# Kernel optimization log

Measured on AMD Instinct MI355X. Metric: run time of the kernel, lower is better.

Reference implementation:

```python
import jax, jax.numpy as jnp
import numpy as np

TOPK = 4
ROUTE_SCALE = 1.0


def setup_inputs() -> dict:
    key = jax.random.key(0)
    ks = jax.random.split(key, 16)
    B, S, C, D = 4, 512, 4, 2048
    E, H = 16, 1408
    SH = 2 * H  # n_shared_experts * moe_inter_dim
    s = 0.02
    return {
        "embeddings": jax.random.normal(ks[0], (B, S, C, D), jnp.float32),
        "x": jax.random.normal(ks[1], (B, S, C, 1), jnp.float32),
        "Wg": jax.random.normal(ks[2], (E, D), jnp.float32) * s,
        "W1": jax.random.normal(ks[3], (E, H, D), jnp.float32) * s,
        "b1": jax.random.normal(ks[4], (E, H), jnp.float32) * s,
        "W2": jax.random.normal(ks[5], (E, D, H), jnp.float32) * s,
        "b2": jax.random.normal(ks[6], (E, D), jnp.float32) * s,
        "W3": jax.random.normal(ks[7], (E, H, D), jnp.float32) * s,
        "b3": jax.random.normal(ks[8], (E, H), jnp.float32) * s,
        "Ws1": jax.random.normal(ks[9], (SH, D), jnp.float32) * s,
        "bs1": jax.random.normal(ks[10], (SH,), jnp.float32) * s,
        "Ws2": jax.random.normal(ks[11], (D, SH), jnp.float32) * s,
        "bs2": jax.random.normal(ks[12], (D,), jnp.float32) * s,
    }


def reference(embeddings, x, Wg, W1, b1, W2, b2, W3, b3, Ws1, bs1, Ws2, bs2):
    # NOTE: in the torch module, the `x` arg is immediately shadowed by
    # embeddings.view(-1, dim); it does not participate in the math.
    D = Wg.shape[1]
    E = Wg.shape[0]
    xt = embeddings.reshape(-1, D)  # [N, D] flattened tokens

    # Gate: softmax scores (fp32), top-k routing; n_groups == 1, no gate bias.
    logits = jnp.einsum("nd,ed->ne", xt, Wg)
    scores = jax.nn.softmax(logits.astype(jnp.float32), axis=-1)  # [N, E]
    topv, idx = jax.lax.top_k(scores, TOPK)  # values == gathered original scores
    weights = (topv * ROUTE_SCALE).astype(xt.dtype)  # [N, K]

    # Expert dispatch/combine. Per-token combined weight for expert e is
    # sum_k weights[n, k] * (idx[n, k] == e); unassigned tokens get weight 0,
    # so masked-dense per-expert SwiGLU reproduces the gather/scatter math.
    y = jnp.zeros_like(xt)
    for e in range(E):
        w_e = jnp.sum(weights * (idx == e).astype(weights.dtype), axis=1)  # [N]
        h = jax.nn.silu(xt @ W1[e].T + b1[e]) * (xt @ W3[e].T + b3[e])  # [N, H]
        y = y + (h @ W2[e].T + b2[e]) * w_e[:, None]

    # Shared experts: Linear -> SiLU -> Linear applied to every token.
    z = jax.nn.silu(xt @ Ws1.T + bs1) @ Ws2.T + bs2

    return (y + z).reshape(embeddings.shape)
```

## Files before the change

kernel.cpp:

```cpp
#include <hip/hip_runtime.h>
#include <stdint.h>

#define N_TOK 8192
#define DIM   2048
#define NEXP  16
#define HID   1408
#define SHID  2816
#define KTOP  4
#define TILEMAX 272

typedef __attribute__((ext_vector_type(8))) short bf16x8;
typedef __attribute__((ext_vector_type(4))) float f32x4;

#define MFMA16(a,b,c) __builtin_amdgcn_mfma_f32_16x16x32_bf16((a),(b),(c),0,0,0)

__device__ __forceinline__ unsigned short f2b(float f){
  unsigned u = __float_as_uint(f);
  return (unsigned short)((u + 0x7fffu + ((u >> 16) & 1u)) >> 16);
}
__device__ __forceinline__ unsigned pk2(float a, float b){
  return (unsigned)f2b(a) | ((unsigned)f2b(b) << 16);
}
__device__ __forceinline__ float bu2f(unsigned hs){ return __uint_as_float(hs << 16); }
__device__ __forceinline__ float siluf(float x){ return x / (1.f + expf(-x)); }
__device__ __forceinline__ f32x4 zero4(){ f32x4 z; z[0]=0.f; z[1]=0.f; z[2]=0.f; z[3]=0.f; return z; }

__device__ __forceinline__ void gll16(const unsigned short* g, unsigned short* l){
  __builtin_amdgcn_global_load_lds(
      (const __attribute__((address_space(1))) void*)g,
      (__attribute__((address_space(3))) void*)l, 16, 0, 0);
}

__global__ __launch_bounds__(256) void k_cvt(const float* __restrict__ s,
                                             unsigned short* __restrict__ d, size_t n4){
  size_t i = (size_t)blockIdx.x*256 + threadIdx.x;
  size_t st = (size_t)gridDim.x*256;
  for (; i < n4; i += st){
    float4 v = ((const float4*)s)[i];
    uint2 q; q.x = pk2(v.x, v.y); q.y = pk2(v.z, v.w);
    ((uint2*)d)[i] = q;
  }
}

__global__ __launch_bounds__(256) void k_gate(const float* __restrict__ X, const float* __restrict__ Wg,
                                              float* __restrict__ topw, int* __restrict__ topi,
                                              int* __restrict__ cnt){
  int lane = threadIdx.x & 63;
  int t = blockIdx.x*4 + (threadIdx.x >> 6);
  const float* xr = X + (size_t)t*DIM;
  float xv[32];
#pragma unroll
  for (int i=0;i<32;i++) xv[i] = xr[i*64 + lane];
  float sc[NEXP];
#pragma unroll
  for (int e=0;e<NEXP;e++){
    const float* wr = Wg + e*DIM;
    float s = 0.f;
#pragma unroll
    for (int i=0;i<32;i++) s = fmaf(xv[i], wr[i*64 + lane], s);
#pragma unroll
    for (int d=1; d<64; d<<=1) s += __shfl_xor(s, d);
    sc[e] = s;
  }
  if (lane == 0){
    float m = sc[0];
#pragma unroll
    for (int e=1;e<NEXP;e++) m = fmaxf(m, sc[e]);
    float den = 0.f;
#pragma unroll
    for (int e=0;e<NEXP;e++){ sc[e] = expf(sc[e]-m); den += sc[e]; }
    float inv = 1.f/den;
#pragma unroll
    for (int e=0;e<NEXP;e++) sc[e] *= inv;
    for (int k=0;k<KTOP;k++){
      int bi = 0; float bv = sc[0];
#pragma unroll
      for (int e=1;e<NEXP;e++) if (sc[e] > bv){ bv = sc[e]; bi = e; }
      topw[t*KTOP+k] = bv;
      topi[t*KTOP+k] = bi;
#pragma unroll
      for (int e=0;e<NEXP;e++) if (e == bi) sc[e] = -1.f;
      atomicAdd(&cnt[bi], 1);
    }
  }
}

__global__ void k_scan(const int* __restrict__ cnt, int* __restrict__ off, int* __restrict__ cur,
                       int* __restrict__ tab){
  if (threadIdx.x == 0){
    int a = 0;
    for (int e=0;e<NEXP;e++){ off[e] = a; cur[e] = a; a += cnt[e]; }
    int n = 0;
    for (int e=0;e<NEXP;e++){
      int nt = (cnt[e] + 127) >> 7;
      for (int r=0;r<nt;r++) tab[n++] = (e << 16) | r;
    }
    for (; n < TILEMAX; ++n) tab[n] = -1;
  }
}

__global__ __launch_bounds__(256) void k_place(const int* __restrict__ topi, const float* __restrict__ topw,
                                               int* __restrict__ cur, int* __restrict__ rows,
                                               float* __restrict__ rw, int* __restrict__ slotL){
  int t = blockIdx.x*256 + threadIdx.x;
#pragma unroll
  for (int k=0;k<KTOP;k++){
    int e = topi[t*KTOP+k];
    int p = atomicAdd(&cur[e], 1);
    rows[p] = t;
    rw[p]   = topw[t*KTOP+k];
    slotL[t*KTOP+k] = p;
  }
}

__device__ __forceinline__ void stage_Bf(unsigned short* lsB, const float* bF,
                                         int ldK, int bn0, int k0, int tid){
#pragma unroll
  for (int j=0;j<8;j++){
    int idx = j*256 + tid, r = idx >> 4, c4 = idx & 15;
    float4 v = *(const float4*)(bF + (size_t)(bn0 + r)*ldK + k0 + c4*4);
    uint2 q; q.x = pk2(v.x, v.y); q.y = pk2(v.z, v.w);
    *(uint2*)&lsB[r*64 + (((c4 >> 1) ^ (r & 7)) << 3) + ((c4 & 1) << 2)] = q;
  }
}

__device__ __forceinline__ void read_A(bf16x8 af[4], const unsigned short* lsA, int wm, int lane, int kc){
  int s = kc*4 + (lane >> 4);
#pragma unroll
  for (int mi=0;mi<4;mi++){
    int r = wm + mi*16 + (lane & 15);
    af[mi] = *(const bf16x8*)&lsA[r*64 + ((s ^ (r & 7)) << 3)];
  }
}

template<bool WBF>
__global__ __launch_bounds__(256,2) void k_g13(const unsigned short* __restrict__ Xb,
    const void* __restrict__ W1p, const void* __restrict__ W3p,
    const float* __restrict__ b1, const float* __restrict__ b3,
    const int* __restrict__ rows, const int* __restrict__ cnt, const int* __restrict__ offs,
    const int* __restrict__ tab, unsigned short* __restrict__ H1)
{
  int bid = blockIdx.x;
  int l = bid >> 3;
  int ct = l / 34;
  int slot = (bid & 7)*34 + (l - ct*34);
  int ent = tab[slot];
  if (ent < 0) return;
  int e = ent >> 16, rt = ent & 0xffff;
  int cntE = cnt[e];
  int offE = offs[e];
  int hn0 = ct*128;
  int tid = threadIdx.x, lane = tid & 63, wid = tid >> 6;
  int wm = (wid >> 1)*64, wn = (wid & 1)*64;
  __shared__ alignas(16) unsigned short lsA[8192], lsB1[8192], lsB3[8192];

  int lr8 = lane >> 3;
  int cx  = (lane & 7) ^ lr8;
  unsigned offA[4];
#pragma unroll
  for (int j=0;j<4;j++){
    int lrow = rt*128 + wid*32 + j*8 + lr8;
    int arow = rows[offE + (lrow < cntE ? lrow : cntE-1)];
    offA[j] = (unsigned)arow*DIM + (unsigned)cx*8;
  }
  unsigned offB0 = (unsigned)(hn0 + wid*32 + lr8)*DIM + (unsigned)cx*8;
  const unsigned short* b1H = (const unsigned short*)W1p + (size_t)e*HID*DIM;
  const unsigned short* b3H = (const unsigned short*)W3p + (size_t)e*HID*DIM;
  const float* b1F = (const float*)W1p + (size_t)e*HID*DIM;
  const float* b3F = (const float*)W3p + (size_t)e*HID*DIM;
  unsigned short* lA  = &lsA[wid*2048];
  unsigned short* lB1 = &lsB1[wid*2048];
  unsigned short* lB3 = &lsB3[wid*2048];

  f32x4 acc1[4][4], acc3[4][4];
#pragma unroll
  for (int i=0;i<4;i++)
#pragma unroll
    for (int j=0;j<4;j++){ acc1[i][j] = zero4(); acc3[i][j] = zero4(); }

  for (int kt=0; kt<DIM/64; ++kt){
    int k0 = kt*64;
    __syncthreads();
#pragma unroll
    for (int j=0;j<4;j++){
      gll16(Xb + offA[j] + k0, lA + j*512);
      if constexpr (WBF){
        gll16(b1H + offB0 + j*(8*DIM) + k0, lB1 + j*512);
        gll16(b3H + offB0 + j*(8*DIM) + k0, lB3 + j*512);
      }
    }
    if constexpr (!WBF){
      stage_Bf(lsB1, b1F, DIM, hn0, k0, tid);
      stage_Bf(lsB3, b3F, DIM, hn0, k0, tid);
    }
    __syncthreads();
#pragma unroll
    for (int kc=0;kc<2;kc++){
      bf16x8 af[4]; read_A(af, lsA, wm, lane, kc);
      int sB = kc*4 + (lane >> 4);
#pragma unroll
      for (int nj=0;nj<4;nj++){
        int rb = wn + nj*16 + (lane & 15);
        int lof = rb*64 + ((sB ^ (rb & 7)) << 3);
        bf16x8 bf1 = *(const bf16x8*)&lsB1[lof];
        bf16x8 bf3 = *(const bf16x8*)&lsB3[lof];
#pragma unroll
        for (int mi=0;mi<4;mi++){
          acc1[mi][nj] = MFMA16(af[mi], bf1, acc1[mi][nj]);
          acc3[mi][nj] = MFMA16(af[mi], bf3, acc3[mi][nj]);
        }
      }
    }
  }
#pragma unroll
  for (int nj=0;nj<4;nj++){
    int h = hn0 + wn + nj*16 + (lane & 15);
    float b1v = b1[e*HID + h];
    float b3v = b3[e*HID + h];
#pragma unroll
    for (int mi=0;mi<4;mi++){
#pragma unroll
      for (int r=0;r<4;r++){
        int gr = rt*128 + wm + mi*16 + (lane >> 4)*4 + r;
        if (gr < cntE){
          float u = acc1[mi][nj][r] + b1v;
          float v = acc3[mi][nj][r] + b3v;
          H1[(size_t)(offE + gr)*HID + h] = f2b(siluf(u)*v);
        }
      }
    }
  }
}

template<int MODE, bool WBF, int KSTEPS>
__global__ __launch_bounds__(256,2) void k_gemm(const unsigned short* __restrict__ Abase,
    const void* __restrict__ Bpv, const float* __restrict__ bias,
    float* __restrict__ outF, unsigned short* __restrict__ outH,
    const int* __restrict__ rows, const float* __restrict__ rw,
    const int* __restrict__ cnt, const int* __restrict__ offs,
    const int* __restrict__ tab)
{
  constexpr int KD = KSTEPS*64;
  int e = 0, ct, rt, cntE = 0, offE = 0;
  int bid = blockIdx.x;
  int l = bid >> 3;
  if constexpr (MODE >= 2){
    ct = l / 34;
    int slot = (bid & 7)*34 + (l - ct*34);
    int ent = tab[slot];
    if (ent < 0) return;
    e = ent >> 16; rt = ent & 0xffff;
    cntE = cnt[e];
    offE = offs[e];
  } else {
    rt = (bid & 7)*8 + (l & 7);
    ct = l >> 3;
  }
  int bn0 = ct*128, t0 = rt*128;
  int tid = threadIdx.x, lane = tid & 63, wid = tid >> 6;
  int wm = (wid >> 1)*64, wn = (wid & 1)*64;
  __shared__ alignas(16) unsigned short lsA[8192], lsB[8192];

  int lr8 = lane >> 3;
  int cx  = (lane & 7) ^ lr8;
  unsigned offA0 = 0;
  unsigned offA[4];
  if constexpr (MODE >= 2){
#pragma unroll
    for (int j=0;j<4;j++){
      int lrow = t0 + wid*32 + j*8 + lr8;
      int arow = offE + (lrow < cntE ? lrow : cntE-1);
      offA[j] = (unsigned)arow*KD + (unsigned)cx*8;
    }
  } else {
    offA0 = (unsigned)(t0 + wid*32 + lr8)*KD + (unsigned)cx*8;
  }
  unsigned offB0 = (unsigned)(bn0 + wid*32 + lr8)*KD + (unsigned)cx*8;
  const unsigned short* bH = (const unsigned short*)Bpv + ((MODE >= 2) ? (size_t)e*2048*KD : (size_t)0);
  const float*          bF = (const float*)Bpv          + ((MODE >= 2) ? (size_t)e*2048*KD : (size_t)0);
  const float* biasp = bias + ((MODE >= 2) ? e*DIM : 0);
  unsigned short* lA = &lsA[wid*2048];
  unsigned short* lB = &lsB[wid*2048];

  f32x4 acc[4][4];
#pragma unroll
  for (int i=0;i<4;i++)
#pragma unroll
    for (int j=0;j<4;j++) acc[i][j] = zero4();

  for (int kt=0; kt<KSTEPS; ++kt){
    int k0 = kt*64;
    __syncthreads();
#pragma unroll
    for (int j=0;j<4;j++){
      if constexpr (MODE >= 2) gll16(Abase + offA[j] + k0, lA + j*512);
      else                     gll16(Abase + offA0 + j*(8*KD) + k0, lA + j*512);
      if constexpr (WBF)       gll16(bH + offB0 + j*(8*KD) + k0, lB + j*512);
    }
    if constexpr (!WBF) stage_Bf(lsB, bF, KD, bn0, k0, tid);
    __syncthreads();
#pragma unroll
    for (int kc=0;kc<2;kc++){
      bf16x8 af[4]; read_A(af, lsA, wm, lane, kc);
      int sB = kc*4 + (lane >> 4);
#pragma unroll
      for (int nj=0;nj<4;nj++){
        int rb = wn + nj*16 + (lane & 15);
        bf16x8 bfr = *(const bf16x8*)&lsB[rb*64 + ((sB ^ (rb & 7)) << 3)];
#pragma unroll
        for (int mi=0;mi<4;mi++)
          acc[mi][nj] = MFMA16(af[mi], bfr, acc[mi][nj]);
      }
    }
  }
#pragma unroll
  for (int nj=0;nj<4;nj++){
    int col = bn0 + wn + nj*16 + (lane & 15);
    float bv = biasp[col];
#pragma unroll
    for (int mi=0;mi<4;mi++){
#pragma unroll
      for (int r=0;r<4;r++){
        int lr = wm + mi*16 + (lane >> 4)*4 + r;
        float v = acc[mi][nj][r] + bv;
        if constexpr (MODE == 0){
          outH[(size_t)(t0 + lr)*SHID + col] = f2b(siluf(v));
        } else if constexpr (MODE == 1){
          outF[(size_t)(t0 + lr)*DIM + col] = v;
        } else {
          int gr = t0 + lr;
          if (gr < cntE){
            int slot = offE + gr;
            float wv = rw[slot] * v;
            if constexpr (MODE == 2){
              atomicAdd(outF + (size_t)rows[slot]*DIM + col, wv);
            } else {
              outH[(size_t)slot*DIM + col] = f2b(wv);
            }
          }
        }
      }
    }
  }
}

__global__ __launch_bounds__(256) void k_comb(const unsigned short* __restrict__ Yr,
                                              const int* __restrict__ slotL, float* __restrict__ out){
  int i = blockIdx.x*256 + threadIdx.x;
  int t = i >> 8, c = i & 255;
  size_t ob = (size_t)t*DIM + (size_t)c*8;
  float4 a = *(float4*)(out + ob);
  float4 b = *(float4*)(out + ob + 4);
  int sl[4];
#pragma unroll
  for (int k=0;k<KTOP;k++) sl[k] = slotL[t*KTOP + k];
#pragma unroll
  for (int k=0;k<KTOP;k++){
    uint4 v = *(const uint4*)(Yr + (size_t)sl[k]*DIM + (size_t)c*8);
    a.x += bu2f(v.x & 0xffffu); a.y += bu2f(v.x >> 16);
    a.z += bu2f(v.y & 0xffffu); a.w += bu2f(v.y >> 16);
    b.x += bu2f(v.z & 0xffffu); b.y += bu2f(v.z >> 16);
    b.z += bu2f(v.w & 0xffffu); b.w += bu2f(v.w >> 16);
  }
  *(float4*)(out + ob) = a;
  *(float4*)(out + ob + 4) = b;
}

extern "C" void kernel_launch(void* const* d_in, const int* in_sizes, int n_in,
                              void* d_out, int out_size, void* d_ws, size_t ws_size,
                              hipStream_t stream)
{
  (void)in_sizes; (void)n_in; (void)out_size;
  const float* emb = (const float*)d_in[0];
  const float* Wg  = (const float*)d_in[2];
  const float* W1  = (const float*)d_in[3];
  const float* b1  = (const float*)d_in[4];
  const float* W2  = (const float*)d_in[5];
  const float* b2  = (const float*)d_in[6];
  const float* W3  = (const float*)d_in[7];
  const float* b3  = (const float*)d_in[8];
  const float* Ws1 = (const float*)d_in[9];
  const float* bs1 = (const float*)d_in[10];
  const float* Ws2 = (const float*)d_in[11];
  const float* bs2 = (const float*)d_in[12];
  float* out = (float*)d_out;
  char* ws = (char*)d_ws;

  const size_t SZ_XB = (size_t)N_TOK*DIM*2;
  const size_t SZ_H1 = (size_t)N_TOK*KTOP*HID*2;
  const size_t SZ_HS = (size_t)N_TOK*SHID*2;
  const size_t SZ_T4 = (size_t)N_TOK*KTOP*4;
  const size_t SZ_WB = (size_t)NEXP*HID*DIM*2;
  const size_t SZ_SB = (size_t)SHID*DIM*2;
  const size_t SZ_YR = (size_t)N_TOK*KTOP*DIM*2;

  size_t off_xb = 0;
  size_t off_h1 = off_xb + SZ_XB;
  size_t off_hs = off_h1 + SZ_H1;
  size_t off_tw = off_hs + SZ_HS;
  size_t off_ti = off_tw + SZ_T4;
  size_t off_ro = off_ti + SZ_T4;
  size_t off_rw = off_ro + SZ_T4;
  size_t off_sl = off_rw + SZ_T4;
  size_t off_cnt = off_sl + SZ_T4;
  size_t off_off = off_cnt + 256;
  size_t off_cur = off_off + 256;
  size_t off_tab = off_cur + 256;
  size_t base_end = off_tab + TILEMAX*4 + 64;
  size_t off_w1b = base_end;
  size_t off_w3b = off_w1b + SZ_WB;
  size_t off_w2b = off_w3b + SZ_WB;
  size_t off_s1b = off_w2b + SZ_WB;
  size_t off_s2b = off_s1b + SZ_SB;
  size_t wbf_end = off_s2b + SZ_SB;

  bool wbf = ws_size >= wbf_end;
  size_t off_yr = wbf ? wbf_end : base_end;
  bool comb = ws_size >= off_yr + SZ_YR;

  unsigned short* Xb = (unsigned short*)(ws + off_xb);
  unsigned short* H1 = (unsigned short*)(ws + off_h1);
  unsigned short* Hs = (unsigned short*)(ws + off_hs);
  float* topw = (float*)(ws + off_tw);
  int*   topi = (int*)(ws + off_ti);
  int*   rowsL= (int*)(ws + off_ro);
  float* rwL  = (float*)(ws + off_rw);
  int*   slotL= (int*)(ws + off_sl);
  int*   cntP = (int*)(ws + off_cnt);
  int*   offP = (int*)(ws + off_off);
  int*   curP = (int*)(ws + off_cur);
  int*   tabP = (int*)(ws + off_tab);
  unsigned short* Yr = (unsigned short*)(ws + off_yr);

  hipMemsetAsync(ws + off_cnt, 0, 768, stream);
  k_cvt<<<2048, 256, 0, stream>>>(emb, Xb, (size_t)N_TOK*DIM/4);
  if (wbf){
    k_cvt<<<2048, 256, 0, stream>>>(W1,  (unsigned short*)(ws + off_w1b), (size_t)NEXP*HID*DIM/4);
    k_cvt<<<2048, 256, 0, stream>>>(W3,  (unsigned short*)(ws + off_w3b), (size_t)NEXP*HID*DIM/4);
    k_cvt<<<2048, 256, 0, stream>>>(W2,  (unsigned short*)(ws + off_w2b), (size_t)NEXP*HID*DIM/4);
    k_cvt<<<512,  256, 0, stream>>>(Ws1, (unsigned short*)(ws + off_s1b), (size_t)SHID*DIM/4);
    k_cvt<<<512,  256, 0, stream>>>(Ws2, (unsigned short*)(ws + off_s2b), (size_t)SHID*DIM/4);
  }
  k_gate<<<2048, 256, 0, stream>>>(emb, Wg, topw, topi, cntP);
  k_scan<<<1, 64, 0, stream>>>(cntP, offP, curP, tabP);
  k_place<<<32, 256, 0, stream>>>(topi, topw, curP, rowsL, rwL, slotL);

  if (wbf) k_g13<true ><<<2992, 256, 0, stream>>>(Xb, ws+off_w1b, ws+off_w3b, b1, b3, rowsL, cntP, offP, tabP, H1);
  else     k_g13<false><<<2992, 256, 0, stream>>>(Xb, W1, W3, b1, b3, rowsL, cntP, offP, tabP, H1);

  if (wbf) k_gemm<0,true ,32><<<1408, 256, 0, stream>>>(Xb, ws+off_s1b, bs1, nullptr, Hs, nullptr,nullptr,nullptr,nullptr,nullptr);
  else     k_gemm<0,false,32><<<1408, 256, 0, stream>>>(Xb, Ws1, bs1, nullptr, Hs, nullptr,nullptr,nullptr,nullptr,nullptr);

  if (wbf) k_gemm<1,true ,44><<<1024, 256, 0, stream>>>(Hs, ws+off_s2b, bs2, out, nullptr, nullptr,nullptr,nullptr,nullptr,nullptr);
  else     k_gemm<1,false,44><<<1024, 256, 0, stream>>>(Hs, Ws2, bs2, out, nullptr, nullptr,nullptr,nullptr,nullptr,nullptr);

  if (comb){
    if (wbf) k_gemm<3,true ,22><<<4352, 256, 0, stream>>>(H1, ws+off_w2b, b2, nullptr, Yr, rowsL, rwL, cntP, offP, tabP);
    else     k_gemm<3,false,22><<<4352, 256, 0, stream>>>(H1, W2, b2, nullptr, Yr, rowsL, rwL, cntP, offP, tabP);
    k_comb<<<N_TOK, 256, 0, stream>>>(Yr, slotL, out);
  } else {
    if (wbf) k_gemm<2,true ,22><<<4352, 256, 0, stream>>>(H1, ws+off_w2b, b2, out, nullptr, rowsL, rwL, cntP, offP, tabP);
    else     k_gemm<2,false,22><<<4352, 256, 0, stream>>>(H1, W2, b2, out, nullptr, rowsL, rwL, cntP, offP, tabP);
  }
}
```

Measured before the change: 1.768 ms.

## Double-buffer LDS staging in expert GEMMs and fuse weight conversion launches

```diff
diff --git a/kernel.cpp b/kernel.cpp
--- a/kernel.cpp
+++ b/kernel.cpp
@@ -39,6 +39,28 @@
     float4 v = ((const float4*)s)[i];
     uint2 q; q.x = pk2(v.x, v.y); q.y = pk2(v.z, v.w);
     ((uint2*)d)[i] = q;
+  }
+}
+
+#define SEGW ((size_t)NEXP*HID*DIM/4)
+#define SEGS ((size_t)SHID*DIM/4)
+__global__ __launch_bounds__(256) void k_cvtW(const float* __restrict__ W1, const float* __restrict__ W3,
+                                              const float* __restrict__ W2, const float* __restrict__ Ws1,
+                                              const float* __restrict__ Ws2,
+                                              unsigned short* __restrict__ d1, unsigned short* __restrict__ d3,
+                                              unsigned short* __restrict__ d2, unsigned short* __restrict__ ds1,
+                                              unsigned short* __restrict__ ds2){
+  size_t total = 3*SEGW + 2*SEGS;
+  for (size_t i = (size_t)blockIdx.x*256 + threadIdx.x; i < total; i += (size_t)gridDim.x*256){
+    const float* s; unsigned short* d; size_t off;
+    if      (i <   SEGW)        { s = W1;  d = d1;  off = i; }
+    else if (i < 2*SEGW)        { s = W3;  d = d3;  off = i - SEGW; }
+    else if (i < 3*SEGW)        { s = W2;  d = d2;  off = i - 2*SEGW; }
+    else if (i < 3*SEGW + SEGS) { s = Ws1; d = ds1; off = i - 3*SEGW; }
+    else                        { s = Ws2; d = ds2; off = i - 3*SEGW - SEGS; }
+    float4 v = ((const float4*)s)[off];
+    uint2 q; q.x = pk2(v.x, v.y); q.y = pk2(v.z, v.w);
+    ((uint2*)d)[off] = q;
   }
 }
 
@@ -124,12 +146,33 @@
   }
 }
 
+__device__ __forceinline__ void stage_Bf32(unsigned short* lsB, const float* bF,
+                                           int bn0, int k0, int tid){
+#pragma unroll
+  for (int j=0;j<4;j++){
+    int idx = j*256 + tid;
+    int r = idx >> 3, c4 = idx & 7;
+    float4 v = *(const float4*)(bF + (size_t)(bn0 + r)*DIM + k0 + c4*4);
+    uint2 q; q.x = pk2(v.x, v.y); q.y = pk2(v.z, v.w);
+    *(uint2*)&lsB[r*32 + (((c4 >> 1) ^ ((r >> 1) & 3)) << 3) + ((c4 & 1) << 2)] = q;
+  }
+}
+
 __device__ __forceinline__ void read_A(bf16x8 af[4], const unsigned short* lsA, int wm, int lane, int kc){
   int s = kc*4 + (lane >> 4);
 #pragma unroll
   for (int mi=0;mi<4;mi++){
     int r = wm + mi*16 + (lane & 15);
     af[mi] = *(const bf16x8*)&lsA[r*64 + ((s ^ (r & 7)) << 3)];
+  }
+}
+
+__device__ __forceinline__ void read_A32(bf16x8 af[4], const unsigned short* lsA, int wm, int lane){
+  int s = lane >> 4;
+#pragma unroll
+  for (int mi=0;mi<4;mi++){
+    int r = wm + mi*16 + (lane & 15);
+    af[mi] = *(const bf16x8*)&lsA[r*32 + ((s ^ ((r >> 1) & 3)) << 3)];
   }
 }
 
@@ -152,25 +195,24 @@
   int hn0 = ct*128;
   int tid = threadIdx.x, lane = tid & 63, wid = tid >> 6;
   int wm = (wid >> 1)*64, wn = (wid & 1)*64;
-  __shared__ alignas(16) unsigned short lsA[8192], lsB1[8192], lsB3[8192];
-
-  int lr8 = lane >> 3;
-  int cx  = (lane & 7) ^ lr8;
-  unsigned offA[4];
-#pragma unroll
-  for (int j=0;j<4;j++){
-    int lrow = rt*128 + wid*32 + j*8 + lr8;
+  __shared__ alignas(16) unsigned short lsA[2][4096], lsB1[2][4096], lsB3[2][4096];
+
+  int r0 = tid >> 2;
+  int sl = tid & 3;
+  int cxg = sl ^ ((r0 >> 1) & 3);
+  unsigned offA[2];
+#pragma unroll
+  for (int j=0;j<2;j++){
+    int lrow = rt*128 + r0 + j*64;
     int arow = rows[offE + (lrow < cntE ? lrow : cntE-1)];
-    offA[j] = (unsigned)arow*DIM + (unsigned)cx*8;
-  }
-  unsigned offB0 = (unsigned)(hn0 + wid*32 + lr8)*DIM + (unsigned)cx*8;
+    offA[j] = (unsigned)arow*DIM + (unsigned)cxg*8;
+  }
+  unsigned offB0 = (unsigned)(hn0 + r0)*DIM + (unsigned)cxg*8;
   const unsigned short* b1H = (const unsigned short*)W1p + (size_t)e*HID*DIM;
   const unsigned short* b3H = (const unsigned short*)W3p + (size_t)e*HID*DIM;
   const float* b1F = (const float*)W1p + (size_t)e*HID*DIM;
   const float* b3F = (const float*)W3p + (size_t)e*HID*DIM;
-  unsigned short* lA  = &lsA[wid*2048];
-  unsigned short* lB1 = &lsB1[wid*2048];
-  unsigned short* lB3 = &lsB3[wid*2048];
+  unsigned dst0 = (unsigned)tid*8;
 
   f32x4 acc1[4][4], acc3[4][4];
 #pragma unroll
@@ -178,39 +220,42 @@
 #pragma unroll
     for (int j=0;j<4;j++){ acc1[i][j] = zero4(); acc3[i][j] = zero4(); }
 
-  for (int kt=0; kt<DIM/64; ++kt){
-    int k0 = kt*64;
+  auto STAGE = [&](int set, int k0){
+#pragma unroll
+    for (int j=0;j<2;j++){
+      gll16(Xb + offA[j] + k0, &lsA[set][dst0 + j*2048]);
+      if constexpr (WBF){
+        gll16(b1H + offB0 + j*(64*DIM) + k0, &lsB1[set][dst0 + j*2048]);
+        gll16(b3H + offB0 + j*(64*DIM) + k0, &lsB3[set][dst0 + j*2048]);
+      }
+    }
+    if constexpr (!WBF){
+      stage_Bf32(lsB1[set], b1F, hn0, k0, tid);
+      stage_Bf32(lsB3[set], b3F, hn0, k0, tid);
+    }
+  };
+
+  STAGE(0, 0);
+  __syncthreads();
+  int cur = 0;
+  for (int kt=0; kt<DIM/32; ++kt){
+    if (kt+1 < DIM/32) STAGE(cur^1, (kt+1)*32);
+    bf16x8 af[4]; read_A32(af, lsA[cur], wm, lane);
+    int s = lane >> 4;
+#pragma unroll
+    for (int nj=0;nj<4;nj++){
+      int rb = wn + nj*16 + (lane & 15);
+      int lof = rb*32 + ((s ^ ((rb >> 1) & 3)) << 3);
+      bf16x8 bf1 = *(const bf16x8*)&lsB1[cur][lof];
+      bf16x8 bf3 = *(const bf16x8*)&lsB3[cur][lof];
+#pragma unroll
+      for (int mi=0;mi<4;mi++){
+        acc1[mi][nj] = MFMA16(af[mi], bf1, acc1[mi][nj]);
+        acc3[mi][nj] = MFMA16(af[mi], bf3, acc3[mi][nj]);
+      }
+    }
     __syncthreads();
-#pragma unroll
-    for (int j=0;j<4;j++){
-      gll16(Xb + offA[j] + k0, lA + j*512);
-      if constexpr (WBF){
-        gll16(b1H + offB0 + j*(8*DIM) + k0, lB1 + j*512);
-        gll16(b3H + offB0 + j*(8*DIM) + k0, lB3 + j*512);
-      }
-    }
-    if constexpr (!WBF){
-      stage_Bf(lsB1, b1F, DIM, hn0, k0, tid);
-      stage_Bf(lsB3, b3F, DIM, hn0, k0, tid);
-    }
-    __syncthreads();
-#pragma unroll
-    for (int kc=0;kc<2;kc++){
-      bf16x8 af[4]; read_A(af, lsA, wm, lane, kc);
-      int sB = kc*4 + (lane >> 4);
-#pragma unroll
-      for (int nj=0;nj<4;nj++){
-        int rb = wn + nj*16 + (lane & 15);
-        int lof = rb*64 + ((sB ^ (rb & 7)) << 3);
-        bf16x8 bf1 = *(const bf16x8*)&lsB1[lof];
-        bf16x8 bf3 = *(const bf16x8*)&lsB3[lof];
-#pragma unroll
-        for (int mi=0;mi<4;mi++){
-          acc1[mi][nj] = MFMA16(af[mi], bf1, acc1[mi][nj]);
-          acc3[mi][nj] = MFMA16(af[mi], bf3, acc3[mi][nj]);
-        }
-      }
-    }
+    cur ^= 1;
   }
 #pragma unroll
   for (int nj=0;nj<4;nj++){
@@ -259,7 +304,7 @@
   int bn0 = ct*128, t0 = rt*128;
   int tid = threadIdx.x, lane = tid & 63, wid = tid >> 6;
   int wm = (wid >> 1)*64, wn = (wid & 1)*64;
-  __shared__ alignas(16) unsigned short lsA[8192], lsB[8192];
+  __shared__ alignas(16) unsigned short lsA[2][8192], lsB[2][8192];
 
   int lr8 = lane >> 3;
   int cx  = (lane & 7) ^ lr8;
@@ -279,8 +324,6 @@
   const unsigned short* bH = (const unsigned short*)Bpv + ((MODE >= 2) ? (size_t)e*2048*KD : (size_t)0);
   const float*          bF = (const float*)Bpv          + ((MODE >= 2) ? (size_t)e*2048*KD : (size_t)0);
   const float* biasp = bias + ((MODE >= 2) ? e*DIM : 0);
-  unsigned short* lA = &lsA[wid*2048];
-  unsigned short* lB = &lsB[wid*2048];
 
   f32x4 acc[4][4];
 #pragma unroll
@@ -288,30 +331,36 @@
 #pragma unroll
     for (int j=0;j<4;j++) acc[i][j] = zero4();
 
+  auto STAGE = [&](int set, int k0){
+#pragma unroll
+    for (int j=0;j<4;j++){
+      if constexpr (MODE >= 2) gll16(Abase + offA[j] + k0, &lsA[set][wid*2048 + j*512]);
+      else                     gll16(Abase + offA0 + j*(8*KD) + k0, &lsA[set][wid*2048 + j*512]);
+      if constexpr (WBF)       gll16(bH + offB0 + j*(8*KD) + k0, &lsB[set][wid*2048 + j*512]);
+    }
+    if constexpr (!WBF) stage_Bf(lsB[set], bF, KD, bn0, k0, tid);
+  };
+
+  STAGE(0, 0);
+  __syncthreads();
+  int cur = 0;
   for (int kt=0; kt<KSTEPS; ++kt){
-    int k0 = kt*64;
-    __syncthreads();
-#pragma unroll
-    for (int j=0;j<4;j++){
-      if constexpr (MODE >= 2) gll16(Abase + offA[j] + k0, lA + j*512);
-      else                     gll16(Abase + offA0 + j*(8*KD) + k0, lA + j*512);
-      if constexpr (WBF)       gll16(bH + offB0 + j*(8*KD) + k0, lB + j*512);
-    }
-    if constexpr (!WBF) stage_Bf(lsB, bF, KD, bn0, k0, tid);
-    __syncthreads();
+    if (kt+1 < KSTEPS) STAGE(cur^1, (kt+1)*64);
 #pragma unroll
     for (int kc=0;kc<2;kc++){
-      bf16x8 af[4]; read_A(af, lsA, wm, lane, kc);
+      bf16x8 af[4]; read_A(af, lsA[cur], wm, lane, kc);
       int sB = kc*4 + (lane >> 4);
 #pragma unroll
       for (int nj=0;nj<4;nj++){
         int rb = wn + nj*16 + (lane & 15);
-        bf16x8 bfr = *(const bf16x8*)&lsB[rb*64 + ((sB ^ (rb & 7)) << 3)];
+        bf16x8 bfr = *(const bf16x8*)&lsB[cur][rb*64 + ((sB ^ (rb & 7)) << 3)];
 #pragma unroll
         for (int mi=0;mi<4;mi++)
           acc[mi][nj] = MFMA16(af[mi], bfr, acc[mi][nj]);
       }
     }
+    __syncthreads();
+    cur ^= 1;
   }
 #pragma unroll
   for (int nj=0;nj<4;nj++){
@@ -435,11 +484,10 @@
   hipMemsetAsync(ws + off_cnt, 0, 768, stream);
   k_cvt<<<2048, 256, 0, stream>>>(emb, Xb, (size_t)N_TOK*DIM/4);
   if (wbf){
-    k_cvt<<<2048, 256, 0, stream>>>(W1,  (unsigned short*)(ws + off_w1b), (size_t)NEXP*HID*DIM/4);
-    k_cvt<<<2048, 256, 0, stream>>>(W3,  (unsigned short*)(ws + off_w3b), (size_t)NEXP*HID*DIM/4);
-    k_cvt<<<2048, 256, 0, stream>>>(W2,  (unsigned short*)(ws + off_w2b), (size_t)NEXP*HID*DIM/4);
-    k_cvt<<<512,  256, 0, stream>>>(Ws1, (unsigned short*)(ws + off_s1b), (size_t)SHID*DIM/4);
-    k_cvt<<<512,  256, 0, stream>>>(Ws2, (unsigned short*)(ws + off_s2b), (size_t)SHID*DIM/4);
+    k_cvtW<<<4096, 256, 0, stream>>>(W1, W3, W2, Ws1, Ws2,
+        (unsigned short*)(ws + off_w1b), (unsigned short*)(ws + off_w3b),
+        (unsigned short*)(ws + off_w2b), (unsigned short*)(ws + off_s1b),
+        (unsigned short*)(ws + off_s2b));
   }
   k_gate<<<2048, 256, 0, stream>>>(emb, Wg, topw, topi, cntP);
   k_scan<<<1, 64, 0, stream>>>(cntP, offP, curP, tabP);
```

New measurement: 2.079 ms. 17.6% more time.

## Widen GEMM N-tile to 256, fuse X conversion into gate, merge weight casts

Applied to the files above, without the earlier changes.

```diff
diff --git a/kernel.cpp b/kernel.cpp
--- a/kernel.cpp
+++ b/kernel.cpp
@@ -31,33 +31,52 @@
       (__attribute__((address_space(3))) void*)l, 16, 0, 0);
 }
 
-__global__ __launch_bounds__(256) void k_cvt(const float* __restrict__ s,
-                                             unsigned short* __restrict__ d, size_t n4){
-  size_t i = (size_t)blockIdx.x*256 + threadIdx.x;
-  size_t st = (size_t)gridDim.x*256;
-  for (; i < n4; i += st){
-    float4 v = ((const float4*)s)[i];
+#define SEGW ((size_t)NEXP*HID*DIM/4)
+#define SEGS ((size_t)SHID*DIM/4)
+__global__ __launch_bounds__(256) void k_cvtW(const float* __restrict__ W1, const float* __restrict__ W3,
+                                              const float* __restrict__ W2, const float* __restrict__ Ws1,
+                                              const float* __restrict__ Ws2,
+                                              unsigned short* __restrict__ d1, unsigned short* __restrict__ d3,
+                                              unsigned short* __restrict__ d2, unsigned short* __restrict__ ds1,
+                                              unsigned short* __restrict__ ds2){
+  size_t total = 3*SEGW + 2*SEGS;
+  for (size_t i = (size_t)blockIdx.x*256 + threadIdx.x; i < total; i += (size_t)gridDim.x*256){
+    const float* s; unsigned short* d; size_t off;
+    if      (i <   SEGW)        { s = W1;  d = d1;  off = i; }
+    else if (i < 2*SEGW)        { s = W3;  d = d3;  off = i - SEGW; }
+    else if (i < 3*SEGW)        { s = W2;  d = d2;  off = i - 2*SEGW; }
+    else if (i < 3*SEGW + SEGS) { s = Ws1; d = ds1; off = i - 3*SEGW; }
+    else                        { s = Ws2; d = ds2; off = i - 3*SEGW - SEGS; }
+    float4 v = ((const float4*)s)[off];
     uint2 q; q.x = pk2(v.x, v.y); q.y = pk2(v.z, v.w);
-    ((uint2*)d)[i] = q;
+    ((uint2*)d)[off] = q;
   }
 }
 
 __global__ __launch_bounds__(256) void k_gate(const float* __restrict__ X, const float* __restrict__ Wg,
                                               float* __restrict__ topw, int* __restrict__ topi,
-                                              int* __restrict__ cnt){
+                                              int* __restrict__ cnt, unsigned short* __restrict__ Xb){
   int lane = threadIdx.x & 63;
   int t = blockIdx.x*4 + (threadIdx.x >> 6);
   const float* xr = X + (size_t)t*DIM;
-  float xv[32];
-#pragma unroll
-  for (int i=0;i<32;i++) xv[i] = xr[i*64 + lane];
+  float4 xv[8];
+#pragma unroll
+  for (int i=0;i<8;i++){
+    xv[i] = *(const float4*)(xr + i*256 + lane*4);
+    uint2 q; q.x = pk2(xv[i].x, xv[i].y); q.y = pk2(xv[i].z, xv[i].w);
+    *(uint2*)(Xb + (size_t)t*DIM + i*256 + lane*4) = q;
+  }
   float sc[NEXP];
 #pragma unroll
   for (int e=0;e<NEXP;e++){
     const float* wr = Wg + e*DIM;
     float s = 0.f;
 #pragma unroll
-    for (int i=0;i<32;i++) s = fmaf(xv[i], wr[i*64 + lane], s);
+    for (int i=0;i<8;i++){
+      float4 w = *(const float4*)(wr + i*256 + lane*4);
+      s = fmaf(xv[i].x, w.x, s); s = fmaf(xv[i].y, w.y, s);
+      s = fmaf(xv[i].z, w.z, s); s = fmaf(xv[i].w, w.w, s);
+    }
 #pragma unroll
     for (int d=1; d<64; d<<=1) s += __shfl_xor(s, d);
     sc[e] = s;
@@ -113,10 +132,11 @@
   }
 }
 
+template<int ROUNDS>
 __device__ __forceinline__ void stage_Bf(unsigned short* lsB, const float* bF,
                                          int ldK, int bn0, int k0, int tid){
 #pragma unroll
-  for (int j=0;j<8;j++){
+  for (int j=0;j<ROUNDS;j++){
     int idx = j*256 + tid, r = idx >> 4, c4 = idx & 15;
     float4 v = *(const float4*)(bF + (size_t)(bn0 + r)*ldK + k0 + c4*4);
     uint2 q; q.x = pk2(v.x, v.y); q.y = pk2(v.z, v.w);
@@ -190,8 +210,8 @@
       }
     }
     if constexpr (!WBF){
-      stage_Bf(lsB1, b1F, DIM, hn0, k0, tid);
-      stage_Bf(lsB3, b3F, DIM, hn0, k0, tid);
+      stage_Bf<8>(lsB1, b1F, DIM, hn0, k0, tid);
+      stage_Bf<8>(lsB3, b3F, DIM, hn0, k0, tid);
     }
     __syncthreads();
 #pragma unroll
@@ -256,10 +276,10 @@
     rt = (bid & 7)*8 + (l & 7);
     ct = l >> 3;
   }
-  int bn0 = ct*128, t0 = rt*128;
+  int bn0 = ct*256, t0 = rt*128;
   int tid = threadIdx.x, lane = tid & 63, wid = tid >> 6;
-  int wm = (wid >> 1)*64, wn = (wid & 1)*64;
-  __shared__ alignas(16) unsigned short lsA[8192], lsB[8192];
+  int wm = (wid >> 1)*64, wn = (wid & 1)*128;
+  __shared__ alignas(16) unsigned short lsA[8192], lsB[16384];
 
   int lr8 = lane >> 3;
   int cx  = (lane & 7) ^ lr8;
@@ -275,18 +295,18 @@
   } else {
     offA0 = (unsigned)(t0 + wid*32 + lr8)*KD + (unsigned)cx*8;
   }
-  unsigned offB0 = (unsigned)(bn0 + wid*32 + lr8)*KD + (unsigned)cx*8;
+  unsigned offB0 = (unsigned)(bn0 + wid*64 + lr8)*KD + (unsigned)cx*8;
   const unsigned short* bH = (const unsigned short*)Bpv + ((MODE >= 2) ? (size_t)e*2048*KD : (size_t)0);
   const float*          bF = (const float*)Bpv          + ((MODE >= 2) ? (size_t)e*2048*KD : (size_t)0);
   const float* biasp = bias + ((MODE >= 2) ? e*DIM : 0);
   unsigned short* lA = &lsA[wid*2048];
-  unsigned short* lB = &lsB[wid*2048];
-
-  f32x4 acc[4][4];
+  unsigned short* lB = &lsB[wid*4096];
+
+  f32x4 acc[4][8];
 #pragma unroll
   for (int i=0;i<4;i++)
 #pragma unroll
-    for (int j=0;j<4;j++) acc[i][j] = zero4();
+    for (int j=0;j<8;j++) acc[i][j] = zero4();
 
   for (int kt=0; kt<KSTEPS; ++kt){
     int k0 = kt*64;
@@ -295,16 +315,20 @@
     for (int j=0;j<4;j++){
       if constexpr (MODE >= 2) gll16(Abase + offA[j] + k0, lA + j*512);
       else                     gll16(Abase + offA0 + j*(8*KD) + k0, lA + j*512);
-      if constexpr (WBF)       gll16(bH + offB0 + j*(8*KD) + k0, lB + j*512);
-    }
-    if constexpr (!WBF) stage_Bf(lsB, bF, KD, bn0, k0, tid);
+    }
+    if constexpr (WBF){
+#pragma unroll
+      for (int j=0;j<8;j++) gll16(bH + offB0 + j*(8*KD) + k0, lB + j*512);
+    } else {
+      stage_Bf<16>(lsB, bF, KD, bn0, k0, tid);
+    }
     __syncthreads();
 #pragma unroll
     for (int kc=0;kc<2;kc++){
       bf16x8 af[4]; read_A(af, lsA, wm, lane, kc);
       int sB = kc*4 + (lane >> 4);
 #pragma unroll
-      for (int nj=0;nj<4;nj++){
+      for (int nj=0;nj<8;nj++){
         int rb = wn + nj*16 + (lane & 15);
         bf16x8 bfr = *(const bf16x8*)&lsB[rb*64 + ((sB ^ (rb & 7)) << 3)];
 #pragma unroll
@@ -314,7 +338,7 @@
     }
   }
 #pragma unroll
-  for (int nj=0;nj<4;nj++){
+  for (int nj=0;nj<8;nj++){
     int col = bn0 + wn + nj*16 + (lane & 15);
     float bv = biasp[col];
 #pragma unroll
@@ -433,33 +457,31 @@
   unsigned short* Yr = (unsigned short*)(ws + off_yr);
 
   hipMemsetAsync(ws + off_cnt, 0, 768, stream);
-  k_cvt<<<2048, 256, 0, stream>>>(emb, Xb, (size_t)N_TOK*DIM/4);
   if (wbf){
-    k_cvt<<<2048, 256, 0, stream>>>(W1,  (unsigned short*)(ws + off_w1b), (size_t)NEXP*HID*DIM/4);
-    k_cvt<<<2048, 256, 0, stream>>>(W3,  (unsigned short*)(ws + off_w3b), (size_t)NEXP*HID*DIM/4);
-    k_cvt<<<2048, 256, 0, stream>>>(W2,  (unsigned short*)(ws + off_w2b), (size_t)NEXP*HID*DIM/4);
-    k_cvt<<<512,  256, 0, stream>>>(Ws1, (unsigned short*)(ws + off_s1b), (size_t)SHID*DIM/4);
-    k_cvt<<<512,  256, 0, stream>>>(Ws2, (unsigned short*)(ws + off_s2b), (size_t)SHID*DIM/4);
-  }
-  k_gate<<<2048, 256, 0, stream>>>(emb, Wg, topw, topi, cntP);
+    k_cvtW<<<4096, 256, 0, stream>>>(W1, W3, W2, Ws1, Ws2,
+        (unsigned short*)(ws + off_w1b), (unsigned short*)(ws + off_w3b),
+        (unsigned short*)(ws + off_w2b), (unsigned short*)(ws + off_s1b),
+        (unsigned short*)(ws + off_s2b));
+  }
+  k_gate<<<2048, 256, 0, stream>>>(emb, Wg, topw, topi, cntP, Xb);
   k_scan<<<1, 64, 0, stream>>>(cntP, offP, curP, tabP);
   k_place<<<32, 256, 0, stream>>>(topi, topw, curP, rowsL, rwL, slotL);
 
   if (wbf) k_g13<true ><<<2992, 256, 0, stream>>>(Xb, ws+off_w1b, ws+off_w3b, b1, b3, rowsL, cntP, offP, tabP, H1);
   else     k_g13<false><<<2992, 256, 0, stream>>>(Xb, W1, W3, b1, b3, rowsL, cntP, offP, tabP, H1);
 
-  if (wbf) k_gemm<0,true ,32><<<1408, 256, 0, stream>>>(Xb, ws+off_s1b, bs1, nullptr, Hs, nullptr,nullptr,nullptr,nullptr,nullptr);
-  else     k_gemm<0,false,32><<<1408, 256, 0, stream>>>(Xb, Ws1, bs1, nullptr, Hs, nullptr,nullptr,nullptr,nullptr,nullptr);
-
-  if (wbf) k_gemm<1,true ,44><<<1024, 256, 0, stream>>>(Hs, ws+off_s2b, bs2, out, nullptr, nullptr,nullptr,nullptr,nullptr,nullptr);
-  else     k_gemm<1,false,44><<<1024, 256, 0, stream>>>(Hs, Ws2, bs2, out, nullptr, nullptr,nullptr,nullptr,nullptr,nullptr);
+  if (wbf) k_gemm<0,true ,32><<<704, 256, 0, stream>>>(Xb, ws+off_s1b, bs1, nullptr, Hs, nullptr,nullptr,nullptr,nullptr,nullptr);
+  else     k_gemm<0,false,32><<<704, 256, 0, stream>>>(Xb, Ws1, bs1, nullptr, Hs, nullptr,nullptr,nullptr,nullptr,nullptr);
+
+  if (wbf) k_gemm<1,true ,44><<<512, 256, 0, stream>>>(Hs, ws+off_s2b, bs2, out, nullptr, nullptr,nullptr,nullptr,nullptr,nullptr);
+  else     k_gemm<1,false,44><<<512, 256, 0, stream>>>(Hs, Ws2, bs2, out, nullptr, nullptr,nullptr,nullptr,nullptr,nullptr);
 
   if (comb){
-    if (wbf) k_gemm<3,true ,22><<<4352, 256, 0, stream>>>(H1, ws+off_w2b, b2, nullptr, Yr, rowsL, rwL, cntP, offP, tabP);
-    else     k_gemm<3,false,22><<<4352, 256, 0, stream>>>(H1, W2, b2, nullptr, Yr, rowsL, rwL, cntP, offP, tabP);
+    if (wbf) k_gemm<3,true ,22><<<2176, 256, 0, stream>>>(H1, ws+off_w2b, b2, nullptr, Yr, rowsL, rwL, cntP, offP, tabP);
+    else     k_gemm<3,false,22><<<2176, 256, 0, stream>>>(H1, W2, b2, nullptr, Yr, rowsL, rwL, cntP, offP, tabP);
     k_comb<<<N_TOK, 256, 0, stream>>>(Yr, slotL, out);
   } else {
-    if (wbf) k_gemm<2,true ,22><<<4352, 256, 0, stream>>>(H1, ws+off_w2b, b2, out, nullptr, rowsL, rwL, cntP, offP, tabP);
-    else     k_gemm<2,false,22><<<4352, 256, 0, stream>>>(H1, W2, b2, out, nullptr, rowsL, rwL, cntP, offP, tabP);
-  }
-}
+    if (wbf) k_gemm<2,true ,22><<<2176, 256, 0, stream>>>(H1, ws+off_w2b, b2, out, nullptr, rowsL, rwL, cntP, offP, tabP);
+    else     k_gemm<2,false,22><<<2176, 256, 0, stream>>>(H1, W2, b2, out, nullptr, rowsL, rwL, cntP, offP, tabP);
+  }
+}
```

New measurement: 1.839 ms. 1.04x slower.
